# Kernel optimization log

Measured on AMD Instinct MI355X. Metric: run time of the kernel, lower is better.

The kernel has to match this reference:

```python
import jax, jax.numpy as jnp
import numpy as np

K = 5  # kNN neighbors (includes self, as in PyG knn(x, x, k))


def _lin_bn(x, W, b, s, h):
    # Linear -> ReLU -> BatchNorm (inference, folded to scale s / shift h)
    return jax.nn.relu(x @ W + b) * s + h


def _knn_idx(x, k):
    # x: [B, N, F] -> idx: [B, N, k] indices of k nearest points (incl. self)
    x2 = jnp.sum(x * x, axis=-1)  # [B, N]
    d = x2[:, :, None] + x2[:, None, :] - 2.0 * jnp.einsum('bnf,bmf->bnm', x, x)
    return jax.lax.top_k(-d, k)[1]


def _edge_conv(x, k, edge_mlp):
    # DynamicEdgeConv: knn graph, message mlp([x_i, x_j - x_i]), max-aggregate
    idx = _knn_idx(x, k)                                   # [B, N, k]
    xj = jax.vmap(lambda xb, ib: xb[ib])(x, idx)           # [B, N, k, F]
    xi = jnp.broadcast_to(x[:, :, None, :], xj.shape)
    e = jnp.concatenate([xi, xj - xi], axis=-1)            # [B, N, k, 2F]
    return jnp.max(edge_mlp(e), axis=2)                    # [B, N, F_out]


def _forward(pos, w1a, b1a, s1a, h1a, w1b, b1b, s1b, h1b, w1c, b1c, s1c, h1c,
             w2, b2, s2, h2, wl, bl, sl, hl,
             wm1, bm1, sm1, hm1, wm2, bm2, sm2, hm2, wout, bout):
    mlp1 = lambda e: _lin_bn(_lin_bn(_lin_bn(e, w1a, b1a, s1a, h1a),
                                     w1b, b1b, s1b, h1b), w1c, b1c, s1c, h1c)
    mlp2 = lambda e: _lin_bn(e, w2, b2, s2, h2)
    x1 = _edge_conv(pos, K, mlp1)                          # [B, N, 64]
    x2 = _edge_conv(x1, K, mlp2)                           # [B, N, 128]
    out = _lin_bn(jnp.concatenate([x1, x2], axis=-1), wl, bl, sl, hl)  # [B,N,1024]
    out = jnp.max(out, axis=1)                             # global max pool -> [B,1024]
    out = _lin_bn(out, wm1, bm1, sm1, hm1)                 # Dropout = identity (eval)
    out = _lin_bn(out, wm2, bm2, sm2, hm2)
    return out @ wout + bout                               # [B, n_classes]


def setup_inputs() -> dict:
    key = jax.random.key(0)
    ks = jax.random.split(key, 32)
    B, N = 32, 2048
    rn = lambda k, sh: jax.random.normal(k, sh, dtype=jnp.float32)
    ru = lambda k, sh: jax.random.uniform(k, sh, dtype=jnp.float32)
    d = {'pos': rn(ks[0], (B, N, 3))}
    i = 1
    for nm, cin, cout in [('1a', 6, 64), ('1b', 64, 64), ('1c', 64, 64),
                          ('2', 128, 128), ('l', 192, 1024),
                          ('m1', 1024, 512), ('m2', 512, 256)]:
        d['w' + nm] = rn(ks[i], (cin, cout)) / np.sqrt(cin); i += 1
        d['b' + nm] = rn(ks[i], (cout,)) * 0.1; i += 1
        d['s' + nm] = ru(ks[i], (cout,)) + 0.5; i += 1
        d['h' + nm] = rn(ks[i], (cout,)) * 0.1; i += 1
    d['wout'] = rn(ks[i], (256, 2)) / np.sqrt(256.0); i += 1
    d['bout'] = rn(ks[i], (2,)) * 0.1
    return d


def reference(pos, w1a, b1a, s1a, h1a, w1b, b1b, s1b, h1b, w1c, b1c, s1c, h1c,
              w2, b2, s2, h2, wl, bl, sl, hl,
              wm1, bm1, sm1, hm1, wm2, bm2, sm2, hm2, wout, bout):
    return _forward(pos, w1a, b1a, s1a, h1a, w1b, b1b, s1b, h1b, w1c, b1c, s1c, h1c,
                    w2, b2, s2, h2, wl, bl, sl, hl,
                    wm1, bm1, sm1, hm1, wm2, bm2, sm2, hm2, wout, bout)
```

## Files before the change

### kernel.cpp

```cpp
#include <hip/hip_runtime.h>

#define DEV __device__ __forceinline__
DEV float relu_(float x) { return fmaxf(x, 0.0f); }

typedef __attribute__((ext_vector_type(4))) float f32x4;
typedef __attribute__((ext_vector_type(8))) __bf16 bf16x8;

DEV unsigned short bfbits(__bf16 b) { union { unsigned short s; __bf16 b; } x; x.b = b; return x.s; }
DEV __bf16 bffrom(unsigned short s) { union { unsigned short s; __bf16 b; } x; x.s = s; return x.b; }

DEV void knn_insert(float (&bd)[5], int (&bi)[5], float d, int j) {
  if (d >= bd[4]) return;
  bd[4] = d; bi[4] = j;
#pragma unroll
  for (int p = 4; p > 0; --p) {
    if (bd[p] < bd[p - 1]) {
      float td = bd[p]; bd[p] = bd[p - 1]; bd[p - 1] = td;
      int ti = bi[p]; bi[p] = bi[p - 1]; bi[p - 1] = ti;
    }
  }
}

DEV void knn_insert_bl(float (&bd)[5], int (&bi)[5], float d, int j) {
#pragma unroll
  for (int p = 0; p < 5; ++p) {
    bool lt = d < bd[p];
    float nd = lt ? d : bd[p];
    float cd = lt ? bd[p] : d;
    int ni = lt ? j : bi[p];
    int ci = lt ? bi[p] : j;
    bd[p] = nd; d = cd;
    bi[p] = ni; j = ci;
  }
}

DEV void ins5(float (&b)[5], float x) {
  b[4] = __builtin_amdgcn_fmed3f(b[3], b[4], x);
  b[3] = __builtin_amdgcn_fmed3f(b[2], b[3], x);
  b[2] = __builtin_amdgcn_fmed3f(b[1], b[2], x);
  b[1] = __builtin_amdgcn_fmed3f(b[0], b[1], x);
  b[0] = fminf(b[0], x);
}

DEV void merge_net5(float (&a)[5], float b0, float b1, float b2, float b3, float b4) {
  float c0 = fminf(a[0], b0);
  float c1 = fminf(fminf(b1, a[1]), fmaxf(a[0], b0));
  float c2 = fminf(fminf(b2, a[2]), fminf(fmaxf(a[0], b1), fmaxf(a[1], b0)));
  float c3 = fminf(fminf(b3, a[3]),
                   fminf(fmaxf(a[0], b2), fminf(fmaxf(a[1], b1), fmaxf(a[2], b0))));
  float c4 = fminf(fminf(b4, a[4]),
                   fminf(fminf(fmaxf(a[0], b3), fmaxf(a[1], b2)),
                         fminf(fmaxf(a[2], b1), fmaxf(a[3], b0))));
  a[0] = c0; a[1] = c1; a[2] = c2; a[3] = c3; a[4] = c4;
}

__global__ __launch_bounds__(256) void k_front(
    const float* __restrict__ pos, const float* __restrict__ w1a,
    const float* __restrict__ b1a, const float* __restrict__ w1b,
    const float* __restrict__ w1c, const float* __restrict__ w2,
    const float* __restrict__ wl,
    int* __restrict__ idx1, float* __restrict__ uR, float* __restrict__ vR,
    __bf16* __restrict__ wfh, __bf16* __restrict__ wfl,
    __bf16* __restrict__ wph, __bf16* __restrict__ wpl,
    __bf16* __restrict__ wlb) {
  __shared__ __align__(16) float smem[9472];
  int tid = threadIdx.x;
  int blk = blockIdx.x;
  if (blk < 2048) {
    float* xs = smem;
    float* sqs = smem + 6144;
    float* md = smem + 8192;
    int* mi = (int*)(smem + 8832);
    int b = blk >> 6, qc = blk & 63;
    const float* src = pos + b * 6144;
    for (int u = tid; u < 6144; u += 256) {
      float v = src[u];
      int p = u / 3, c = u - p * 3;
      smem[c * 2048 + p] = v;
    }
    __syncthreads();
    for (int u = tid; u < 2048; u += 256) {
      float x = xs[u], y = xs[2048 + u], z = xs[4096 + u];
      sqs[u] = fmaf(z, z, fmaf(y, y, x * x));
    }
    __syncthreads();
    int q = tid & 31, sub = tid >> 5;
    int qi = qc * 32 + q;
    float qx = xs[qi], qy = xs[2048 + qi], qz = xs[4096 + qi];
    float qsq = sqs[qi];
    float bp[5] = {1e30f, 1e30f, 1e30f, 1e30f, 1e30f};
    int j0 = sub * 256;
    for (int j4 = 0; j4 < 64; ++j4) {
      int jb = j0 + j4 * 4;
      float4 xv = *(const float4*)(xs + jb);
      float4 yv = *(const float4*)(xs + 2048 + jb);
      float4 zv = *(const float4*)(xs + 4096 + jb);
      float4 sv = *(const float4*)(sqs + jb);
      float xa[4] = {xv.x, xv.y, xv.z, xv.w};
      float ya[4] = {yv.x, yv.y, yv.z, yv.w};
      float za[4] = {zv.x, zv.y, zv.z, zv.w};
      float sa[4] = {sv.x, sv.y, sv.z, sv.w};
#pragma unroll
      for (int c = 0; c < 4; ++c) {
        float dot = fmaf(qz, za[c], fmaf(qy, ya[c], qx * xa[c]));
        float d = fmaxf((qsq + sa[c]) - 2.0f * dot, 0.0f);
        unsigned u = (__float_as_uint(d) & 0xFFFFFF00u) | (unsigned)(j4 * 4 + c);
        ins5(bp, __uint_as_float(u));
      }
    }
    float bd[5]; int bi[5];
#pragma unroll
    for (int k = 0; k < 5; ++k) {
      unsigned u = __float_as_uint(bp[k]);
      bd[k] = __uint_as_float(u & 0xFFFFFF00u);
      bi[k] = j0 + (int)(u & 255u);
    }
    for (int half = 4; half >= 1; half >>= 1) {
      __syncthreads();
      if (sub >= half && sub < 2 * half) {
        int slot = (q * 4 + (sub - half)) * 5;
#pragma unroll
        for (int k = 0; k < 5; ++k) { md[slot + k] = bd[k]; mi[slot + k] = bi[k]; }
      }
      __syncthreads();
      if (sub < half) {
        int slot = (q * 4 + sub) * 5;
#pragma unroll
        for (int k = 0; k < 5; ++k) knn_insert_bl(bd, bi, md[slot + k], mi[slot + k]);
      }
    }
    if (sub == 0) {
      int* op = idx1 + (b * 2048 + qi) * 5;
#pragma unroll
      for (int k = 0; k < 5; ++k) op[k] = bi[k];
    }
  } else if (blk < 3072) {
    float* wAs = smem;
    float* bs = smem + 384;
    float* uS = smem + 448;
    float* vS = smem + 4800;
    for (int u = tid; u < 384; u += 256) wAs[u] = w1a[u];
    if (tid < 64) bs[tid] = b1a[tid];
    __syncthreads();
    int lane = tid & 63, fq = tid >> 6;
    int p0 = (blk - 2048) * 64;
    int p = p0 + lane;
    float x0 = pos[p * 3], x1 = pos[p * 3 + 1], x2 = pos[p * 3 + 2];
#pragma unroll
    for (int m = 0; m < 16; ++m) {
      int f = fq * 16 + m;
      float wt0 = wAs[f], wt1 = wAs[64 + f], wt2 = wAs[128 + f];
      float wb0 = wAs[192 + f], wb1 = wAs[256 + f], wb2 = wAs[320 + f];
      float uval = bs[f];
      uval = fmaf(x0, wt0 - wb0, uval);
      uval = fmaf(x1, wt1 - wb1, uval);
      uval = fmaf(x2, wt2 - wb2, uval);
      uS[lane * 68 + f] = uval;
      vS[lane * 68 + f] = fmaf(x2, wb2, fmaf(x1, wb1, x0 * wb0));
    }
    __syncthreads();
#pragma unroll
    for (int it = 0; it < 4; ++it) {
      int g = it * 1024 + tid * 4;
      int pl = g >> 6, f = g & 63;
      float4 uu = *(const float4*)(uS + pl * 68 + f);
      float4 vv = *(const float4*)(vS + pl * 68 + f);
      *(float4*)(uR + (size_t)p0 * 64 + g) = uu;
      *(float4*)(vR + (size_t)p0 * 64 + g) = vv;
    }
  } else {
    int pblk = blk - 3072;
    if (pblk < 4) {
      int t = pblk * 256 + tid;
      int m = t >> 9;
      int rem = t & 511;
      int nb = rem >> 7;
      int rem2 = rem & 127;
      int s = rem2 >> 6, lane = rem2 & 63;
      int k0 = s * 32 + (lane >> 4) * 8;
      int c = nb * 16 + (lane & 15);
      const float* W = m ? w1c : w1b;
      __bf16 oh[8], ol[8];
#pragma unroll
      for (int j = 0; j < 8; ++j) {
        float val = W[(k0 + j) * 64 + c];
        __bf16 h = (__bf16)val;
        oh[j] = h;
        ol[j] = (__bf16)(val - (float)h);
      }
      size_t off = (size_t)m * 4096 + ((size_t)((nb * 2 + s) * 64 + lane)) * 8;
      *(uint4*)(wfh + off) = *(const uint4*)oh;
      *(uint4*)(wfl + off) = *(const uint4*)ol;
    } else if (pblk < 12) {
      int t = (pblk - 4) * 256 + tid;
      int nb = t >> 7;
      int rem = t & 127;
      int ks = rem >> 6, lane = rem & 63;
      int k0 = ks * 32 + (lane >> 4) * 8;
      int col16 = lane & 15;
      __bf16 oh[8], ol[8];
#pragma unroll
      for (int j = 0; j < 8; ++j) {
        int k = k0 + j;
        float val;
        if (nb < 8) {
          int c = nb * 16 + col16;
          val = w2[k * 128 + c] - w2[(64 + k) * 128 + c];
        } else {
          int c = (nb - 8) * 16 + col16;
          val = w2[(64 + k) * 128 + c];
        }
        __bf16 h = (__bf16)val;
        oh[j] = h;
        ol[j] = (__bf16)(val - (float)h);
      }
      *(uint4*)(wph + (size_t)t * 8) = *(const uint4*)oh;
      *(uint4*)(wpl + (size_t)t * 8) = *(const uint4*)ol;
    } else {
      int t = (pblk - 12) * 256 + tid;
      int nt = t / 3072;
      int rem = t - nt * 3072;
      int ks = rem / 512;
      int rem2 = rem - ks * 512;
      int nb = rem2 >> 6, lane = rem2 & 63;
      int k0 = ks * 32 + (lane >> 4) * 8;
      int n = nt * 128 + nb * 16 + (lane & 15);
      __bf16 o[8];
#pragma unroll
      for (int j = 0; j < 8; ++j) o[j] = (__bf16)wl[(k0 + j) * 1024 + n];
      *(uint4*)(wlb + (size_t)t * 8) = *(const uint4*)o;
    }
  }
}

__global__ __launch_bounds__(256) void k_edge1(
    const int* __restrict__ idx1, const float* __restrict__ uR,
    const float* __restrict__ vR,
    const float* __restrict__ s1a, const float* __restrict__ h1a,
    const float* __restrict__ b1b, const float* __restrict__ s1b,
    const float* __restrict__ h1b,
    const float* __restrict__ b1c, const float* __restrict__ s1c,
    const float* __restrict__ h1c,
    const __bf16* __restrict__ wfh, const __bf16* __restrict__ wfl,
    __bf16* __restrict__ xh, __bf16* __restrict__ xl,
    float* __restrict__ sqo, __bf16* __restrict__ xb) {
  __shared__ __align__(16) __bf16 Wh[8192], Wl[8192];
  __shared__ __align__(16) unsigned h2b[4 * 1088];
  int tid = threadIdx.x;
  int w = tid >> 6, lane = tid & 63;
  int quad = lane >> 4, lm = lane & 15;
#pragma unroll
  for (int it = 0; it < 4; ++it) {
    int u4 = it * 256 + tid;
    *(uint4*)(Wh + (size_t)u4 * 8) = *(const uint4*)(wfh + (size_t)u4 * 8);
    *(uint4*)(Wl + (size_t)u4 * 8) = *(const uint4*)(wfl + (size_t)u4 * 8);
  }
  int p0 = blockIdx.x * 64;
  int b = p0 >> 11;
  size_t bb = (size_t)b * 2048;
  int edge = p0 + w * 16 + lm;
  float sA[2][8], hA[2][8];
#pragma unroll
  for (int s = 0; s < 2; ++s)
#pragma unroll
    for (int j = 0; j < 8; ++j) {
      int k = s * 32 + quad * 8 + j;
      sA[s][j] = s1a[k]; hA[s][j] = h1a[k];
    }
  float bB[4], sB[4], hB[4], bC[4], sC[4], hC[4];
#pragma unroll
  for (int nb = 0; nb < 4; ++nb) {
    int c = nb * 16 + lm;
    bB[nb] = b1b[c]; sB[nb] = s1b[c]; hB[nb] = h1b[c];
    bC[nb] = b1c[c]; sC[nb] = s1c[c]; hC[nb] = h1c[c];
  }
  unsigned* h2w = h2b + w * 1088;
  f32x4 mmax[4];
#pragma unroll
  for (int nb = 0; nb < 4; ++nb)
    mmax[nb] = (f32x4){-3.4e38f, -3.4e38f, -3.4e38f, -3.4e38f};
  __syncthreads();
  const float* urow = uR + (size_t)edge * 64;
  for (int kk = 0; kk < 5; ++kk) {
    int jn = idx1[edge * 5 + kk];
    const float* vrow = vR + (bb + jn) * 64;
    bf16x8 Ah[2], Al[2];
#pragma unroll
    for (int s = 0; s < 2; ++s) {
      int off = s * 32 + quad * 8;
      float4 u0 = *(const float4*)(urow + off);
      float4 u1 = *(const float4*)(urow + off + 4);
      float4 v0 = *(const float4*)(vrow + off);
      float4 v1 = *(const float4*)(vrow + off + 4);
      float uv[8] = {u0.x + v0.x, u0.y + v0.y, u0.z + v0.z, u0.w + v0.w,
                     u1.x + v1.x, u1.y + v1.y, u1.z + v1.z, u1.w + v1.w};
      __bf16 th[8], tl[8];
#pragma unroll
      for (int j = 0; j < 8; ++j) {
        float val = relu_(uv[j]) * sA[s][j] + hA[s][j];
        __bf16 hb = (__bf16)val;
        th[j] = hb;
        tl[j] = (__bf16)(val - (float)hb);
      }
      Ah[s] = *(const bf16x8*)th;
      Al[s] = *(const bf16x8*)tl;
    }
#pragma unroll
    for (int nb = 0; nb < 4; ++nb) {
      bf16x8 Bh0 = *(const bf16x8*)(Wh + ((size_t)((nb * 2 + 0) * 64 + lane)) * 8);
      bf16x8 Bh1 = *(const bf16x8*)(Wh + ((size_t)((nb * 2 + 1) * 64 + lane)) * 8);
      bf16x8 Bl0 = *(const bf16x8*)(Wl + ((size_t)((nb * 2 + 0) * 64 + lane)) * 8);
      bf16x8 Bl1 = *(const bf16x8*)(Wl + ((size_t)((nb * 2 + 1) * 64 + lane)) * 8);
      f32x4 a2 = {0.f, 0.f, 0.f, 0.f};
      a2 = __builtin_amdgcn_mfma_f32_16x16x32_bf16(Ah[0], Bh0, a2, 0, 0, 0);
      a2 = __builtin_amdgcn_mfma_f32_16x16x32_bf16(Ah[1], Bh1, a2, 0, 0, 0);
      a2 = __builtin_amdgcn_mfma_f32_16x16x32_bf16(Ah[0], Bl0, a2, 0, 0, 0);
      a2 = __builtin_amdgcn_mfma_f32_16x16x32_bf16(Ah[1], Bl1, a2, 0, 0, 0);
      a2 = __builtin_amdgcn_mfma_f32_16x16x32_bf16(Al[0], Bh0, a2, 0, 0, 0);
      a2 = __builtin_amdgcn_mfma_f32_16x16x32_bf16(Al[1], Bh1, a2, 0, 0, 0);
#pragma unroll
      for (int r = 0; r < 4; ++r) {
        float vv2 = relu_(a2[r] + bB[nb]) * sB[nb] + hB[nb];
        __bf16 hb = (__bf16)vv2;
        __bf16 lb = (__bf16)(vv2 - (float)hb);
        h2w[(quad * 4 + r) * 68 + nb * 16 + lm] =
            (unsigned)bfbits(hb) | ((unsigned)bfbits(lb) << 16);
      }
    }
    bf16x8 A3h[2], A3l[2];
#pragma unroll
    for (int s = 0; s < 2; ++s) {
      const unsigned* rp = h2w + lm * 68 + s * 32 + quad * 8;
      uint4 da = *(const uint4*)rp;
      uint4 db = *(const uint4*)(rp + 4);
      unsigned dw[8] = {da.x, da.y, da.z, da.w, db.x, db.y, db.z, db.w};
      __bf16 th[8], tl[8];
#pragma unroll
      for (int j = 0; j < 8; ++j) {
        th[j] = bffrom((unsigned short)(dw[j] & 0xFFFFu));
        tl[j] = bffrom((unsigned short)(dw[j] >> 16));
      }
      A3h[s] = *(const bf16x8*)th;
      A3l[s] = *(const bf16x8*)tl;
    }
#pragma unroll
    for (int nb = 0; nb < 4; ++nb) {
      bf16x8 Bh0 = *(const bf16x8*)(Wh + 4096 + ((size_t)((nb * 2 + 0) * 64 + lane)) * 8);
      bf16x8 Bh1 = *(const bf16x8*)(Wh + 4096 + ((size_t)((nb * 2 + 1) * 64 + lane)) * 8);
      bf16x8 Bl0 = *(const bf16x8*)(Wl + 4096 + ((size_t)((nb * 2 + 0) * 64 + lane)) * 8);
      bf16x8 Bl1 = *(const bf16x8*)(Wl + 4096 + ((size_t)((nb * 2 + 1) * 64 + lane)) * 8);
      f32x4 a3 = {0.f, 0.f, 0.f, 0.f};
      a3 = __builtin_amdgcn_mfma_f32_16x16x32_bf16(A3h[0], Bh0, a3, 0, 0, 0);
      a3 = __builtin_amdgcn_mfma_f32_16x16x32_bf16(A3h[1], Bh1, a3, 0, 0, 0);
      a3 = __builtin_amdgcn_mfma_f32_16x16x32_bf16(A3h[0], Bl0, a3, 0, 0, 0);
      a3 = __builtin_amdgcn_mfma_f32_16x16x32_bf16(A3h[1], Bl1, a3, 0, 0, 0);
      a3 = __builtin_amdgcn_mfma_f32_16x16x32_bf16(A3l[0], Bh0, a3, 0, 0, 0);
      a3 = __builtin_amdgcn_mfma_f32_16x16x32_bf16(A3l[1], Bh1, a3, 0, 0, 0);
#pragma unroll
      for (int r = 0; r < 4; ++r) mmax[nb][r] = fmaxf(mmax[nb][r], a3[r]);
    }
  }
  float sqp[4] = {0.f, 0.f, 0.f, 0.f};
#pragma unroll
  for (int nb = 0; nb < 4; ++nb) {
    int c = nb * 16 + lm;
#pragma unroll
    for (int r = 0; r < 4; ++r) {
      float vv3 = relu_(mmax[nb][r] + bC[nb]) * sC[nb] + hC[nb];
      sqp[r] = fmaf(vv3, vv3, sqp[r]);
      __bf16 hb = (__bf16)vv3;
      __bf16 lb = (__bf16)(vv3 - (float)hb);
      int n = p0 + w * 16 + quad * 4 + r;
      xh[(size_t)n * 64 + c] = hb;
      xl[(size_t)n * 64 + c] = lb;
      xb[(size_t)n * 192 + c] = hb;
    }
  }
#pragma unroll
  for (int r = 0; r < 4; ++r) {
    float s = sqp[r];
    s += __shfl_xor(s, 1);
    s += __shfl_xor(s, 2);
    s += __shfl_xor(s, 4);
    s += __shfl_xor(s, 8);
    if (lm == 0) sqo[p0 + w * 16 + quad * 4 + r] = s;
  }
}

__global__ __launch_bounds__(256) void k_mid(const __bf16* __restrict__ xh,
                                             const __bf16* __restrict__ xl,
                                             const float* __restrict__ sq,
                                             __bf16* __restrict__ scratch,
                                             const __bf16* __restrict__ wph,
                                             const __bf16* __restrict__ wpl,
                                             __bf16* __restrict__ Pb,
                                             __bf16* __restrict__ Qb) {
  __shared__ __align__(16) float smem[6656];
  int tid = threadIdx.x;
  int w = tid >> 6, lane = tid & 63;
  int quad = lane >> 4, lm = lane & 15;
  if (blockIdx.x < 1024) {
    __bf16* Bh = (__bf16*)smem;
    __bf16* Bl = (__bf16*)(smem + 2304);
    float* sqs = smem + 4608;
    int blk = blockIdx.x;
    int b = blk >> 5;
    int w5 = blk & 31;
    int qc = w5 >> 1, g = w5 & 1;
    int q0 = qc * 128;
    size_t bb = (size_t)b * 2048;
    for (int u = tid; u < 512; u += 256)
      *(float4*)(sqs + u * 4) = *(const float4*)(sq + bb + u * 4);
    const __bf16* qh0 = xh + (bb + q0 + w * 32 + lm) * 64 + quad * 8;
    const __bf16* ql0 = xl + (bb + q0 + w * 32 + lm) * 64 + quad * 8;
    bf16x8 Ah0a = *(const bf16x8*)(qh0);
    bf16x8 Ah1a = *(const bf16x8*)(qh0 + 32);
    bf16x8 Al0a = *(const bf16x8*)(ql0);
    bf16x8 Al1a = *(const bf16x8*)(ql0 + 32);
    bf16x8 Ah0b = *(const bf16x8*)(qh0 + 1024);
    bf16x8 Ah1b = *(const bf16x8*)(qh0 + 1056);
    bf16x8 Al0b = *(const bf16x8*)(ql0 + 1024);
    bf16x8 Al1b = *(const bf16x8*)(ql0 + 1056);
    int nu = tid >> 3, cu = tid & 7;
    const __bf16* ph0 = xh + (bb + (size_t)g * 1024 + nu) * 64 + cu * 8;
    const __bf16* pl0 = xl + (bb + (size_t)g * 1024 + nu) * 64 + cu * 8;
    __bf16* dh0 = Bh + nu * 72 + cu * 8;
    __bf16* dh1 = Bh + (nu + 32) * 72 + cu * 8;
    __bf16* dl0 = Bl + nu * 72 + cu * 8;
    __bf16* dl1 = Bl + (nu + 32) * 72 + cu * 8;
    uint4 rh0 = *(const uint4*)(ph0);
    uint4 rh1 = *(const uint4*)(ph0 + 2048);
    uint4 rl0 = *(const uint4*)(pl0);
    uint4 rl1 = *(const uint4*)(pl0 + 2048);
    __syncthreads();
    float qsq[8];
#pragma unroll
    for (int r = 0; r < 4; ++r) {
      qsq[r] = sqs[q0 + w * 32 + quad * 4 + r];
      qsq[4 + r] = sqs[q0 + w * 32 + 16 + quad * 4 + r];
    }
    float bp[8][5];
#pragma unroll
    for (int r = 0; r < 8; ++r)
#pragma unroll
      for (int k = 0; k < 5; ++k) bp[r][k] = 1e30f;
    for (int it = 0; it < 16; ++it) {
      *(uint4*)dh0 = rh0;
      *(uint4*)dh1 = rh1;
      *(uint4*)dl0 = rl0;
      *(uint4*)dl1 = rl1;
      __syncthreads();
      if (it < 15) {
        const __bf16* p1 = ph0 + (it + 1) * 4096;
        const __bf16* p2 = pl0 + (it + 1) * 4096;
        rh0 = *(const uint4*)(p1);
        rh1 = *(const uint4*)(p1 + 2048);
        rl0 = *(const uint4*)(p2);
        rl1 = *(const uint4*)(p2 + 2048);
      }
      int ct = g * 16 + it;
#pragma unroll
      for (int nt = 0; nt < 4; ++nt) {
        const __bf16* bph = Bh + (nt * 16 + lm) * 72 + quad * 8;
        const __bf16* bpl = Bl + (nt * 16 + lm) * 72 + quad * 8;
        bf16x8 Bh0 = *(const bf16x8*)(bph);
        bf16x8 Bh1 = *(const bf16x8*)(bph + 32);
        bf16x8 Bl0 = *(const bf16x8*)(bpl);
        bf16x8 Bl1 = *(const bf16x8*)(bpl + 32);
        f32x4 acc0 = {0.f, 0.f, 0.f, 0.f};
        acc0 = __builtin_amdgcn_mfma_f32_16x16x32_bf16(Ah0a, Bh0, acc0, 0, 0, 0);
        acc0 = __builtin_amdgcn_mfma_f32_16x16x32_bf16(Ah1a, Bh1, acc0, 0, 0, 0);
        acc0 = __builtin_amdgcn_mfma_f32_16x16x32_bf16(Ah0a, Bl0, acc0, 0, 0, 0);
        acc0 = __builtin_amdgcn_mfma_f32_16x16x32_bf16(Ah1a, Bl1, acc0, 0, 0, 0);
        acc0 = __builtin_amdgcn_mfma_f32_16x16x32_bf16(Al0a, Bh0, acc0, 0, 0, 0);
        acc0 = __builtin_amdgcn_mfma_f32_16x16x32_bf16(Al1a, Bh1, acc0, 0, 0, 0);
        f32x4 acc1 = {0.f, 0.f, 0.f, 0.f};
        acc1 = __builtin_amdgcn_mfma_f32_16x16x32_bf16(Ah0b, Bh0, acc1, 0, 0, 0);
        acc1 = __builtin_amdgcn_mfma_f32_16x16x32_bf16(Ah1b, Bh1, acc1, 0, 0, 0);
        acc1 = __builtin_amdgcn_mfma_f32_16x16x32_bf16(Ah0b, Bl0, acc1, 0, 0, 0);
        acc1 = __builtin_amdgcn_mfma_f32_16x16x32_bf16(Ah1b, Bl1, acc1, 0, 0, 0);
        acc1 = __builtin_amdgcn_mfma_f32_16x16x32_bf16(Al0b, Bh0, acc1, 0, 0, 0);
        acc1 = __builtin_amdgcn_mfma_f32_16x16x32_bf16(Al1b, Bh1, acc1, 0, 0, 0);
        float csq = sqs[ct * 64 + nt * 16 + lm];
        unsigned key = (unsigned)(it * 4 + nt);
#pragma unroll
        for (int r = 0; r < 4; ++r) {
          float d0 = fmaxf((qsq[r] + csq) - 2.0f * acc0[r], 0.0f);
          unsigned u0 = (__float_as_uint(d0) & 0xFFFFFFC0u) | key;
          ins5(bp[r], __uint_as_float(u0));
          float d1 = fmaxf((qsq[4 + r] + csq) - 2.0f * acc1[r], 0.0f);
          unsigned u1 = (__float_as_uint(d1) & 0xFFFFFFC0u) | key;
          ins5(bp[4 + r], __uint_as_float(u1));
        }
      }
      __syncthreads();
    }
#pragma unroll
    for (int r = 0; r < 8; ++r)
#pragma unroll
      for (int k = 0; k < 5; ++k) {
        unsigned u = __float_as_uint(bp[r][k]);
        bp[r][k] = __uint_as_float((u & 0xFFFFFF00u) | ((u & 63u) << 2) |
                                   (unsigned)(lm & 3));
      }
#pragma unroll
    for (int m = 1; m <= 2; m <<= 1) {
#pragma unroll
      for (int r = 0; r < 8; ++r) {
        float b0 = __shfl_xor(bp[r][0], m);
        float b1 = __shfl_xor(bp[r][1], m);
        float b2 = __shfl_xor(bp[r][2], m);
        float b3 = __shfl_xor(bp[r][3], m);
        float b4 = __shfl_xor(bp[r][4], m);
        merge_net5(bp[r], b0, b1, b2, b3, b4);
      }
    }
    int lmb = lm & ~3;
#pragma unroll
    for (int s = 0; s < 2; ++s) {
      float bd[4][5];
      int bi[4][5];
#pragma unroll
      for (int r = 0; r < 4; ++r)
#pragma unroll
        for (int k = 0; k < 5; ++k) {
          unsigned u = __float_as_uint(bp[s * 4 + r][k]);
          bd[r][k] = __uint_as_float(u & 0xFFFFFF00u);
          unsigned k8 = u & 255u;
          bi[r][k] = (g << 10) | (((int)(k8 >> 2)) << 4) | (lmb | (int)(k8 & 3));
        }
#pragma unroll
      for (int m = 4; m <= 8; m <<= 1) {
#pragma unroll
        for (int r = 0; r < 4; ++r) {
          float od[5]; int oi[5];
#pragma unroll
          for (int k = 0; k < 5; ++k) {
            od[k] = __shfl_xor(bd[r][k], m);
            oi[k] = __shfl_xor(bi[r][k], m);
          }
#pragma unroll
          for (int k = 0; k < 5; ++k) knn_insert(bd[r], bi[r], od[k], oi[k]);
        }
      }
      if (lm == 0) {
#pragma unroll
        for (int r = 0; r < 4; ++r) {
          int qi = q0 + w * 32 + s * 16 + quad * 4 + r;
          uint2* sp = (uint2*)((char*)scratch + (size_t)(bb + qi) * 384 + 128 + g * 40);
#pragma unroll
          for (int k = 0; k < 5; ++k) {
            uint2 v;
            v.x = __float_as_uint(bd[r][k]);
            v.y = (unsigned)bi[r][k];
            sp[k] = v;
          }
        }
      }
    }
  } else {
    __bf16* Wh = (__bf16*)smem;
    __bf16* Wl = (__bf16*)(smem + 2048);
    int n0 = (blockIdx.x - 1024) * 64;
    const __bf16* ah = xh + (size_t)(n0 + w * 16 + lm) * 64 + quad * 8;
    const __bf16* al = xl + (size_t)(n0 + w * 16 + lm) * 64 + quad * 8;
    bf16x8 Ah0 = *(const bf16x8*)(ah);
    bf16x8 Ah1 = *(const bf16x8*)(ah + 32);
    bf16x8 Al0 = *(const bf16x8*)(al);
    bf16x8 Al1 = *(const bf16x8*)(al + 32);
    for (int chunk = 0; chunk < 4; ++chunk) {
      __syncthreads();
#pragma unroll
      for (int it = 0; it < 2; ++it) {
        int unit = it * 256 + tid;
        *(uint4*)(Wh + (size_t)unit * 8) =
            *(const uint4*)(wph + (size_t)chunk * 4096 + (size_t)unit * 8);
        *(uint4*)(Wl + (size_t)unit * 8) =
            *(const uint4*)(wpl + (size_t)chunk * 4096 + (size_t)unit * 8);
      }
      __syncthreads();
#pragma unroll
      for (int nb4 = 0; nb4 < 4; ++nb4) {
        int nb = chunk * 4 + nb4;
        bf16x8 Bh0 = *(const bf16x8*)(Wh + ((size_t)(nb4 * 2 + 0) * 64 + lane) * 8);
        bf16x8 Bh1 = *(const bf16x8*)(Wh + ((size_t)(nb4 * 2 + 1) * 64 + lane) * 8);
        bf16x8 Bl0 = *(const bf16x8*)(Wl + ((size_t)(nb4 * 2 + 0) * 64 + lane) * 8);
        bf16x8 Bl1 = *(const bf16x8*)(Wl + ((size_t)(nb4 * 2 + 1) * 64 + lane) * 8);
        f32x4 acc = {0.f, 0.f, 0.f, 0.f};
        acc = __builtin_amdgcn_mfma_f32_16x16x32_bf16(Ah0, Bh0, acc, 0, 0, 0);
        acc = __builtin_amdgcn_mfma_f32_16x16x32_bf16(Ah1, Bh1, acc, 0, 0, 0);
        acc = __builtin_amdgcn_mfma_f32_16x16x32_bf16(Ah0, Bl0, acc, 0, 0, 0);
        acc = __builtin_amdgcn_mfma_f32_16x16x32_bf16(Ah1, Bl1, acc, 0, 0, 0);
        acc = __builtin_amdgcn_mfma_f32_16x16x32_bf16(Al0, Bh0, acc, 0, 0, 0);
        acc = __builtin_amdgcn_mfma_f32_16x16x32_bf16(Al1, Bh1, acc, 0, 0, 0);
        bool isP = (nb < 8);
        __bf16* base = isP ? Pb : Qb;
        int col = (isP ? nb : nb - 8) * 16 + lm;
#pragma unroll
        for (int r = 0; r < 4; ++r) {
          int n = n0 + w * 16 + quad * 4 + r;
          base[(size_t)n * 128 + col] = (__bf16)acc[r];
        }
      }
    }
  }
}

__global__ __launch_bounds__(256) void k_kmerge(const __bf16* __restrict__ scratch,
                                                int* __restrict__ idx2) {
  int n = blockIdx.x * 256 + threadIdx.x;
  const uint2* sp = (const uint2*)((const char*)scratch + (size_t)n * 384 + 128);
  float bd[5]; int bi[5];
#pragma unroll
  for (int k = 0; k < 5; ++k) {
    uint2 v = sp[k];
    bd[k] = __uint_as_float(v.x);
    bi[k] = (int)v.y;
  }
#pragma unroll
  for (int k = 0; k < 5; ++k) {
    uint2 v = sp[5 + k];
    knn_insert(bd, bi, __uint_as_float(v.x), (int)v.y);
  }
  int* op = idx2 + (size_t)n * 5;
#pragma unroll
  for (int k = 0; k < 5; ++k) op[k] = bi[k];
}

__global__ __launch_bounds__(256) void k_gmax(const __bf16* __restrict__ Pb,
                                              const __bf16* __restrict__ Qb,
                                              const int* __restrict__ idx2,
                                              const float* __restrict__ b2,
                                              const float* __restrict__ s2,
                                              const float* __restrict__ h2v,
                                              __bf16* __restrict__ xb) {
  int tid = threadIdx.x;
  int c4 = tid & 31, p = tid >> 5;
  int n = blockIdx.x * 8 + p;
  int b = n >> 11;
  const int* ip = idx2 + n * 5;
  int c0 = c4 * 4;
  float m[4] = {-3.4e38f, -3.4e38f, -3.4e38f, -3.4e38f};
#pragma unroll
  for (int k = 0; k < 5; ++k) {
    int j = ip[k];
    uint2 q = *(const uint2*)(Qb + ((size_t)(b * 2048 + j)) * 128 + c0);
    m[0] = fmaxf(m[0], (float)bffrom((unsigned short)(q.x & 0xFFFFu)));
    m[1] = fmaxf(m[1], (float)bffrom((unsigned short)(q.x >> 16)));
    m[2] = fmaxf(m[2], (float)bffrom((unsigned short)(q.y & 0xFFFFu)));
    m[3] = fmaxf(m[3], (float)bffrom((unsigned short)(q.y >> 16)));
  }
  uint2 pv = *(const uint2*)(Pb + (size_t)n * 128 + c0);
  float pvf[4] = {(float)bffrom((unsigned short)(pv.x & 0xFFFFu)),
                  (float)bffrom((unsigned short)(pv.x >> 16)),
                  (float)bffrom((unsigned short)(pv.y & 0xFFFFu)),
                  (float)bffrom((unsigned short)(pv.y >> 16))};
  __bf16 o[4];
#pragma unroll
  for (int i = 0; i < 4; ++i) {
    float v = pvf[i] + m[i] + b2[c0 + i];
    o[i] = (__bf16)(relu_(v) * s2[c0 + i] + h2v[c0 + i]);
  }
  uint2 ov;
  ov.x = (unsigned)bfbits(o[0]) | ((unsigned)bfbits(o[1]) << 16);
  ov.y = (unsigned)bfbits(o[2]) | ((unsigned)bfbits(o[3]) << 16);
  *(uint2*)(xb + (size_t)n * 192 + 64 + c0) = ov;
}

__global__ __launch_bounds__(256) void k_linl_mfma(const __bf16* __restrict__ xb,
                                                   const __bf16* __restrict__ wlb,
                                                   float* __restrict__ pool_part) {
  __shared__ __align__(16) __bf16 Aall[12288];
  __shared__ __align__(16) __bf16 Bl[8192];
  int tid = threadIdx.x;
  int w = tid >> 6, lane = tid & 63;
  int mg = blockIdx.x;
  int n0 = mg << 6;
  int quad = lane >> 4, lm = lane & 15;
#pragma unroll
  for (int it = 0; it < 6; ++it) {
    int unit = it * 256 + tid;
    int mb = unit / 384;
    int rem = unit - mb * 384;
    int ks = rem >> 6, ln = rem & 63;
    int lmm = ln & 15, qd = ln >> 4;
    const uint4* ga = (const uint4*)(xb + (size_t)(n0 + mb * 16 + lmm) * 192 + ks * 32 + qd * 8);
    *(uint4*)(Aall + ((size_t)(mb * 6 + ks) * 64 + ln) * 8) = *ga;
  }
  for (int ng = 0; ng < 4; ++ng) {
    f32x4 acc[4][4];
#pragma unroll
    for (int i = 0; i < 4; ++i)
#pragma unroll
      for (int j = 0; j < 4; ++j) acc[i][j] = (f32x4){0.f, 0.f, 0.f, 0.f};
    for (int ks = 0; ks < 6; ++ks) {
      __syncthreads();
#pragma unroll
      for (int nt2 = 0; nt2 < 2; ++nt2) {
#pragma unroll
        for (int u = 0; u < 2; ++u) {
          int unit = u * 256 + tid;
          const uint4* gb = (const uint4*)(wlb + ((size_t)((ng * 2 + nt2) * 6 + ks)) * 4096 + (size_t)unit * 8);
          *(uint4*)(Bl + (size_t)nt2 * 4096 + (size_t)unit * 8) = *gb;
        }
      }
      __syncthreads();
      bf16x8 af[4], bfr[4];
#pragma unroll
      for (int i = 0; i < 4; ++i)
        af[i] = *(const bf16x8*)(Aall + ((size_t)(i * 6 + ks) * 64 + lane) * 8);
      int nt2 = w >> 1, nbb = (w & 1) * 4;
#pragma unroll
      for (int j = 0; j < 4; ++j)
        bfr[j] = *(const bf16x8*)(Bl + (size_t)nt2 * 4096 + ((size_t)((nbb + j) * 64 + lane)) * 8);
#pragma unroll
      for (int i = 0; i < 4; ++i)
#pragma unroll
        for (int j = 0; j < 4; ++j)
          acc[i][j] = __builtin_amdgcn_mfma_f32_16x16x32_bf16(af[i], bfr[j], acc[i][j], 0, 0, 0);
    }
#pragma unroll
    for (int j = 0; j < 4; ++j) {
      float m = -3.4e38f;
#pragma unroll
      for (int i = 0; i < 4; ++i)
#pragma unroll
        for (int r = 0; r < 4; ++r) m = fmaxf(m, acc[i][j][r]);
      m = fmaxf(m, __shfl_xor(m, 16));
      m = fmaxf(m, __shfl_xor(m, 32));
      if (quad == 0) {
        int ch = ng * 256 + (w >> 1) * 128 + (w & 1) * 64 + j * 16 + lm;
        pool_part[(size_t)mg * 1024 + ch] = m;
      }
    }
  }
}

__global__ __launch_bounds__(256) void k_pool(const float* __restrict__ pool_part,
                                              const float* __restrict__ bl,
                                              const float* __restrict__ sl,
                                              const float* __restrict__ hl,
                                              float* __restrict__ p,
                                              float* __restrict__ out) {
  int b = blockIdx.x >> 2, cb = blockIdx.x & 3;
  int c = cb * 256 + threadIdx.x;
  const float* src = pool_part + (size_t)(b * 32) * 1024 + c;
  float m0 = -3.4e38f, m1 = -3.4e38f, m2 = -3.4e38f, m3 = -3.4e38f;
#pragma unroll
  for (int t = 0; t < 32; t += 4) {
    m0 = fmaxf(m0, src[(size_t)t * 1024]);
    m1 = fmaxf(m1, src[(size_t)(t + 1) * 1024]);
    m2 = fmaxf(m2, src[(size_t)(t + 2) * 1024]);
    m3 = fmaxf(m3, src[(size_t)(t + 3) * 1024]);
  }
  float m = fmaxf(fmaxf(m0, m1), fmaxf(m2, m3));
  p[b * 1024 + c] = relu_(m + bl[c]) * sl[c] + hl[c];
  if (blockIdx.x == 0 && threadIdx.x < 64) out[threadIdx.x] = 0.0f;
}

__global__ __launch_bounds__(256) void k_m1(const float* __restrict__ p,
                                            const float* __restrict__ wm1,
                                            const float* __restrict__ bm1,
                                            const float* __restrict__ sm1,
                                            const float* __restrict__ hm1,
                                            float* __restrict__ h1) {
  __shared__ float p_s[1024];
  __shared__ float red[4][64];
  int b = blockIdx.x >> 3, cb = blockIdx.x & 7;
  int tid = threadIdx.x;
  for (int u = tid; u < 1024; u += 256) p_s[u] = p[b * 1024 + u];
  __syncthreads();
  int c64 = tid & 63, q = tid >> 6;
  int C = cb * 64 + c64;
  int f0 = q * 256;
  const float* W = wm1 + (size_t)f0 * 512 + C;
  float a[8] = {0.f, 0.f, 0.f, 0.f, 0.f, 0.f, 0.f, 0.f};
  for (int f = 0; f < 256; f += 8) {
#pragma unroll
    for (int u = 0; u < 8; ++u)
      a[u] = fmaf(p_s[f0 + f + u], W[(size_t)(f + u) * 512], a[u]);
  }
  red[q][c64] = ((a[0] + a[1]) + (a[2] + a[3])) + ((a[4] + a[5]) + (a[6] + a[7]));
  __syncthreads();
  if (tid < 64) {
    float t = (red[0][tid] + red[1][tid]) + (red[2][tid] + red[3][tid]);
    int C2 = cb * 64 + tid;
    h1[b * 512 + C2] = relu_(t + bm1[C2]) * sm1[C2] + hm1[C2];
  }
}

__global__ __launch_bounds__(256) void k_m2o(const float* __restrict__ h1,
                                             const float* __restrict__ wm2,
                                             const float* __restrict__ bm2,
                                             const float* __restrict__ sm2,
                                             const float* __restrict__ hm2,
                                             const float* __restrict__ wout,
                                             const float* __restrict__ bout,
                                             float* __restrict__ out) {
  __shared__ float h1_s[512];
  __shared__ float red[4][64];
  int b = blockIdx.x >> 2, cb = blockIdx.x & 3;
  int tid = threadIdx.x;
  for (int u = tid; u < 512; u += 256) h1_s[u] = h1[b * 512 + u];
  __syncthreads();
  int c64 = tid & 63, q = tid >> 6;
  int C = cb * 64 + c64;
  int f0 = q * 128;
  const float* W = wm2 + (size_t)f0 * 256 + C;
  float a[4] = {0.f, 0.f, 0.f, 0.f};
  for (int f = 0; f < 128; f += 4) {
#pragma unroll
    for (int u = 0; u < 4; ++u)
      a[u] = fmaf(h1_s[f0 + f + u], W[(size_t)(f + u) * 256], a[u]);
  }
  red[q][c64] = (a[0] + a[1]) + (a[2] + a[3]);
  __syncthreads();
  if (tid < 64) {
    float t = (red[0][tid] + red[1][tid]) + (red[2][tid] + red[3][tid]);
    int C2 = cb * 64 + tid;
    float h2v = relu_(t + bm2[C2]) * sm2[C2] + hm2[C2];
    float2 wv = *(const float2*)(wout + C2 * 2);
    float v0 = h2v * wv.x, v1 = h2v * wv.y;
#pragma unroll
    for (int m = 1; m < 64; m <<= 1) {
      v0 += __shfl_xor(v0, m);
      v1 += __shfl_xor(v1, m);
    }
    if (tid == 0) {
      if (cb == 0) { v0 += bout[0]; v1 += bout[1]; }
      atomicAdd(&out[b * 2], v0);
      atomicAdd(&out[b * 2 + 1], v1);
    }
  }
}

extern "C" void kernel_launch(void* const* d_in, const int* in_sizes, int n_in,
                              void* d_out, int out_size, void* d_ws, size_t ws_size,
                              hipStream_t stream) {
  const float* pos = (const float*)d_in[0];
  const float* w1a = (const float*)d_in[1];
  const float* b1a = (const float*)d_in[2];
  const float* s1a = (const float*)d_in[3];
  const float* h1a = (const float*)d_in[4];
  const float* w1b = (const float*)d_in[5];
  const float* b1b = (const float*)d_in[6];
  const float* s1b = (const float*)d_in[7];
  const float* h1b = (const float*)d_in[8];
  const float* w1c = (const float*)d_in[9];
  const float* b1c = (const float*)d_in[10];
  const float* s1c = (const float*)d_in[11];
  const float* h1c = (const float*)d_in[12];
  const float* w2 = (const float*)d_in[13];
  const float* b2 = (const float*)d_in[14];
  const float* s2 = (const float*)d_in[15];
  const float* h2 = (const float*)d_in[16];
  const float* wl = (const float*)d_in[17];
  const float* bl = (const float*)d_in[18];
  const float* sl = (const float*)d_in[19];
  const float* hl = (const float*)d_in[20];
  const float* wm1 = (const float*)d_in[21];
  const float* bm1 = (const float*)d_in[22];
  const float* sm1 = (const float*)d_in[23];
  const float* hm1 = (const float*)d_in[24];
  const float* wm2 = (const float*)d_in[25];
  const float* bm2 = (const float*)d_in[26];
  const float* sm2 = (const float*)d_in[27];
  const float* hm2 = (const float*)d_in[28];
  const float* wout = (const float*)d_in[29];
  const float* bout = (const float*)d_in[30];
  float* out = (float*)d_out;

  float* base = (float*)d_ws;
  __bf16* xh = (__bf16*)base;
  __bf16* xl = (__bf16*)(base + 2097152);
  float* PbF = base + 4194304;
  float* QbF = PbF + 4194304;
  float* xbF = QbF + 4194304;
  int* idx = (int*)(xbF + 6291456);
  float* sq = (float*)(idx + 327680);
  __bf16* wph = (__bf16*)(sq + 65536);
  __bf16* wpl = (__bf16*)(sq + 65536 + 8192);
  __bf16* wfh = (__bf16*)(sq + 65536 + 16384);
  __bf16* wfl = (__bf16*)(sq + 65536 + 20480);
  __bf16* wlb = (__bf16*)(sq + 65536 + 24576);
  __bf16* Pb = (__bf16*)PbF;
  __bf16* Qb = (__bf16*)QbF;
  __bf16* xb = (__bf16*)xbF;
  float* uR = PbF;
  float* vR = QbF;
  float* pool_part = base + 131072;
  float* p_pool = base + 1179648;
  float* h1g = base + 1212416;

  k_front<<<3180, 256, 0, stream>>>(pos, w1a, b1a, w1b, w1c, w2, wl, idx, uR, vR,
                                    wfh, wfl, wph, wpl, wlb);
  k_edge1<<<1024, 256, 0, stream>>>(idx, uR, vR, s1a, h1a, b1b, s1b, h1b, b1c,
                                    s1c, h1c, wfh, wfl, xh, xl, sq, xb);
  k_mid<<<2048, 256, 0, stream>>>(xh, xl, sq, xb, wph, wpl, Pb, Qb);
  k_kmerge<<<256, 256, 0, stream>>>(xb, idx);
  k_gmax<<<8192, 256, 0, stream>>>(Pb, Qb, idx, b2, s2, h2, xb);
  k_linl_mfma<<<1024, 256, 0, stream>>>(xb, wlb, pool_part);
  k_pool<<<128, 256, 0, stream>>>(pool_part, bl, sl, hl, p_pool, out);
  k_m1<<<256, 256, 0, stream>>>(p_pool, wm1, bm1, sm1, hm1, h1g);
  k_m2o<<<128, 256, 0, stream>>>(h1g, wm2, bm2, sm2, hm2, wout, bout, out);
}
```

Measured before the change: 366.4 us.

## Split kNN candidate range four ways and fuse partial-list merge into gmax

The kNN part of k_mid now splits each query tile's candidate points into four groups of 512 instead of two groups of 1024. This doubles the number of kNN blocks and halves the serial loop length in each. The separate k_kmerge kernel is removed. Instead, one lane per point in k_gmax merges the four partial top-5 lists from scratch and broadcasts the indices by shuffle. This removes a launch and the round trip through the idx buffer, at the cost of more partial lists to merge and a serial merge on one lane per point.

Result: slower. 385.1 us (+5.1%).

```diff
diff --git a/kernel.cpp b/kernel.cpp
--- a/kernel.cpp
+++ b/kernel.cpp
@@ -399,14 +399,14 @@
   int tid = threadIdx.x;
   int w = tid >> 6, lane = tid & 63;
   int quad = lane >> 4, lm = lane & 15;
-  if (blockIdx.x < 1024) {
+  if (blockIdx.x < 2048) {
     __bf16* Bh = (__bf16*)smem;
     __bf16* Bl = (__bf16*)(smem + 2304);
     float* sqs = smem + 4608;
     int blk = blockIdx.x;
-    int b = blk >> 5;
-    int w5 = blk & 31;
-    int qc = w5 >> 1, g = w5 & 1;
+    int b = blk >> 6;
+    int w6 = blk & 63;
+    int qc = w6 >> 2, g = w6 & 3;
     int q0 = qc * 128;
     size_t bb = (size_t)b * 2048;
     for (int u = tid; u < 512; u += 256)
@@ -422,8 +422,8 @@
     bf16x8 Al0b = *(const bf16x8*)(ql0 + 1024);
     bf16x8 Al1b = *(const bf16x8*)(ql0 + 1056);
     int nu = tid >> 3, cu = tid & 7;
-    const __bf16* ph0 = xh + (bb + (size_t)g * 1024 + nu) * 64 + cu * 8;
-    const __bf16* pl0 = xl + (bb + (size_t)g * 1024 + nu) * 64 + cu * 8;
+    const __bf16* ph0 = xh + (bb + (size_t)g * 512 + nu) * 64 + cu * 8;
+    const __bf16* pl0 = xl + (bb + (size_t)g * 512 + nu) * 64 + cu * 8;
     __bf16* dh0 = Bh + nu * 72 + cu * 8;
     __bf16* dh1 = Bh + (nu + 32) * 72 + cu * 8;
     __bf16* dl0 = Bl + nu * 72 + cu * 8;
@@ -444,13 +444,13 @@
     for (int r = 0; r < 8; ++r)
 #pragma unroll
       for (int k = 0; k < 5; ++k) bp[r][k] = 1e30f;
-    for (int it = 0; it < 16; ++it) {
+    for (int it = 0; it < 8; ++it) {
       *(uint4*)dh0 = rh0;
       *(uint4*)dh1 = rh1;
       *(uint4*)dl0 = rl0;
       *(uint4*)dl1 = rl1;
       __syncthreads();
-      if (it < 15) {
+      if (it < 7) {
         const __bf16* p1 = ph0 + (it + 1) * 4096;
         const __bf16* p2 = pl0 + (it + 1) * 4096;
         rh0 = *(const uint4*)(p1);
@@ -458,7 +458,7 @@
         rl0 = *(const uint4*)(p2);
         rl1 = *(const uint4*)(p2 + 2048);
       }
-      int ct = g * 16 + it;
+      int ct = g * 8 + it;
 #pragma unroll
       for (int nt = 0; nt < 4; ++nt) {
         const __bf16* bph = Bh + (nt * 16 + lm) * 72 + quad * 8;
@@ -527,7 +527,7 @@
           unsigned u = __float_as_uint(bp[s * 4 + r][k]);
           bd[r][k] = __uint_as_float(u & 0xFFFFFF00u);
           unsigned k8 = u & 255u;
-          bi[r][k] = (g << 10) | (((int)(k8 >> 2)) << 4) | (lmb | (int)(k8 & 3));
+          bi[r][k] = (g << 9) | (((int)(k8 >> 2)) << 4) | (lmb | (int)(k8 & 3));
         }
 #pragma unroll
       for (int m = 4; m <= 8; m <<= 1) {
@@ -561,7 +561,7 @@
   } else {
     __bf16* Wh = (__bf16*)smem;
     __bf16* Wl = (__bf16*)(smem + 2048);
-    int n0 = (blockIdx.x - 1024) * 64;
+    int n0 = (blockIdx.x - 2048) * 64;
     const __bf16* ah = xh + (size_t)(n0 + w * 16 + lm) * 64 + quad * 8;
     const __bf16* al = xl + (size_t)(n0 + w * 16 + lm) * 64 + quad * 8;
     bf16x8 Ah0 = *(const bf16x8*)(ah);
@@ -606,39 +606,42 @@
   }
 }
 
-__global__ __launch_bounds__(256) void k_kmerge(const __bf16* __restrict__ scratch,
-                                                int* __restrict__ idx2) {
-  int n = blockIdx.x * 256 + threadIdx.x;
-  const uint2* sp = (const uint2*)((const char*)scratch + (size_t)n * 384 + 128);
-  float bd[5]; int bi[5];
-#pragma unroll
-  for (int k = 0; k < 5; ++k) {
-    uint2 v = sp[k];
-    bd[k] = __uint_as_float(v.x);
-    bi[k] = (int)v.y;
-  }
-#pragma unroll
-  for (int k = 0; k < 5; ++k) {
-    uint2 v = sp[5 + k];
-    knn_insert(bd, bi, __uint_as_float(v.x), (int)v.y);
-  }
-  int* op = idx2 + (size_t)n * 5;
-#pragma unroll
-  for (int k = 0; k < 5; ++k) op[k] = bi[k];
-}
-
 __global__ __launch_bounds__(256) void k_gmax(const __bf16* __restrict__ Pb,
                                               const __bf16* __restrict__ Qb,
-                                              const int* __restrict__ idx2,
                                               const float* __restrict__ b2,
                                               const float* __restrict__ s2,
                                               const float* __restrict__ h2v,
-                                              __bf16* __restrict__ xb) {
+                                              __bf16* xb) {
   int tid = threadIdx.x;
   int c4 = tid & 31, p = tid >> 5;
   int n = blockIdx.x * 8 + p;
   int b = n >> 11;
-  const int* ip = idx2 + n * 5;
+  int ip0 = 0, ip1 = 0, ip2 = 0, ip3 = 0, ip4 = 0;
+  if (c4 == 0) {
+    const uint2* sp = (const uint2*)((const char*)xb + (size_t)n * 384 + 128);
+    float bd[5]; int bi[5];
+#pragma unroll
+    for (int k = 0; k < 5; ++k) {
+      uint2 v = sp[k];
+      bd[k] = __uint_as_float(v.x);
+      bi[k] = (int)v.y;
+    }
+#pragma unroll
+    for (int gg = 1; gg < 4; ++gg)
+#pragma unroll
+      for (int k = 0; k < 5; ++k) {
+        uint2 v = sp[gg * 5 + k];
+        knn_insert(bd, bi, __uint_as_float(v.x), (int)v.y);
+      }
+    ip0 = bi[0]; ip1 = bi[1]; ip2 = bi[2]; ip3 = bi[3]; ip4 = bi[4];
+  }
+  int src = tid & 32;
+  ip0 = __shfl(ip0, src);
+  ip1 = __shfl(ip1, src);
+  ip2 = __shfl(ip2, src);
+  ip3 = __shfl(ip3, src);
+  ip4 = __shfl(ip4, src);
+  int ip[5] = {ip0, ip1, ip2, ip3, ip4};
   int c0 = c4 * 4;
   float m[4] = {-3.4e38f, -3.4e38f, -3.4e38f, -3.4e38f};
 #pragma unroll
@@ -896,9 +899,8 @@
                                     wfh, wfl, wph, wpl, wlb);
   k_edge1<<<1024, 256, 0, stream>>>(idx, uR, vR, s1a, h1a, b1b, s1b, h1b, b1c,
                                     s1c, h1c, wfh, wfl, xh, xl, sq, xb);
-  k_mid<<<2048, 256, 0, stream>>>(xh, xl, sq, xb, wph, wpl, Pb, Qb);
-  k_kmerge<<<256, 256, 0, stream>>>(xb, idx);
-  k_gmax<<<8192, 256, 0, stream>>>(Pb, Qb, idx, b2, s2, h2, xb);
+  k_mid<<<3072, 256, 0, stream>>>(xh, xl, sq, xb, wph, wpl, Pb, Qb);
+  k_gmax<<<8192, 256, 0, stream>>>(Pb, Qb, b2, s2, h2, xb);
   k_linl_mfma<<<1024, 256, 0, stream>>>(xb, wlb, pool_part);
   k_pool<<<128, 256, 0, stream>>>(pool_part, bl, sl, hl, p_pool, out);
   k_m1<<<256, 256, 0, stream>>>(p_pool, wm1, bm1, sm1, hm1, h1g);
```
